# Performance work log

Measured on AMD Instinct MI355X. Metric: run time of the kernel, lower is better.

The kernel has to match this reference:

```python
import jax, jax.numpy as jnp
import numpy as np

B, S, D_IN, D_K, D_OUT = 8, 2048, 1024, 64, 64

def setup_inputs() -> dict:
    key = jax.random.key(0)
    k1, k2, k3, k4 = jax.random.split(key, 4)
    sc = 1.0 / np.sqrt(D_IN)
    return {
        "X": jax.random.normal(k1, (B, S, D_IN), dtype=jnp.float32),
        "Wq": jax.random.normal(k2, (D_IN, D_K), dtype=jnp.float32) * sc,
        "Wk": jax.random.normal(k3, (D_IN, D_K), dtype=jnp.float32) * sc,
        "Wv": jax.random.normal(k4, (D_IN, D_OUT), dtype=jnp.float32) * sc,
    }

def reference(X, Wq, Wk, Wv):
    # projections (no bias)
    Q = jnp.einsum('bsd,dk->bsk', X, Wq)   # [B,S,d_k]
    K = jnp.einsum('bsd,dk->bsk', X, Wk)   # [B,S,d_k]
    V = jnp.einsum('bsd,dv->bsv', X, Wv)   # [B,S,d_out]
    d_k = Q.shape[-1]
    S_mat = jnp.einsum('bqk,bsk->bqs', Q, K) / jnp.sqrt(jnp.float32(d_k))
    # causal mask: positions j > i get -inf
    causal = jnp.tril(jnp.ones((X.shape[1], X.shape[1]), dtype=bool))
    S_mat = jnp.where(causal[None, :, :], S_mat, -jnp.inf)
    A = jax.nn.softmax(S_mat, axis=-1)
    return jnp.einsum('bqs,bsv->bqv', A, V)
```

## Files before the change

kernel.cpp:

```cpp
#include <hip/hip_runtime.h>
#include <hip/hip_bf16.h>
#include <cstdint>
#include <cstddef>

#define BATCH 8
#define SEQ   2048
#define DIN   1024

typedef float f32x4 __attribute__((ext_vector_type(4)));
typedef float f32x8 __attribute__((ext_vector_type(8)));
typedef __bf16 bf16x8 __attribute__((ext_vector_type(8)));
typedef unsigned short ushort8_t __attribute__((ext_vector_type(8)));

__device__ __forceinline__ unsigned short bfu(float f) {
  __bf16 h = (__bf16)f;
  return __builtin_bit_cast(unsigned short, h);
}

__device__ __forceinline__ bf16x8 cvt8pair(float4 a, float4 b) {
  f32x8 v;
  v[0] = a.x; v[1] = a.y; v[2] = a.z; v[3] = a.w;
  v[4] = b.x; v[5] = b.y; v[6] = b.z; v[7] = b.w;
  return __builtin_convertvector(v, bf16x8);
}

__global__ void pack_w(const float* __restrict__ Wq, const float* __restrict__ Wk,
                       const float* __restrict__ Wv, unsigned short* __restrict__ Wp) {
  const int t = blockIdx.x * blockDim.x + threadIdx.x;
  const int lane = t & 63;
  const int grp = t >> 6;
  const int ks = grp & 31;
  const int nt = grp >> 5;
  const int n = nt * 16 + (lane & 15);
  const int k0 = ks * 32 + ((lane >> 4) << 3);
  const float* W;
  int col;
  float scale = 1.0f;
  if (n < 64)       { W = Wq; col = n;       scale = 0.125f; }
  else if (n < 128) { W = Wk; col = n - 64;  }
  else              { W = Wv; col = n - 128; }
  ushort8_t out;
#pragma unroll
  for (int j = 0; j < 8; ++j)
    out[j] = bfu(W[(size_t)(k0 + j) * 64 + col] * scale);
  reinterpret_cast<ushort8_t*>(Wp)[t] = out;
}

__global__ __launch_bounds__(256) void qkv_gemm(
    const float* __restrict__ X, const unsigned short* __restrict__ Wp,
    unsigned short* __restrict__ Qb, unsigned short* __restrict__ Kb,
    unsigned short* __restrict__ Vt) {
  __shared__ ushort8_t Af[2048];

  const int tid = threadIdx.x;
  const int lane = tid & 63;
  const int wave = tid >> 6;
  const int l15 = lane & 15;
  const int quad = lane >> 4;
  const int m0 = blockIdx.x * 32;
  const int nt0 = wave * 3;

  const int sr = tid >> 3;
  const int sk = tid & 7;
  const float* xrow = X + (size_t)(m0 + sr) * DIN;

  const ushort8_t* wp = reinterpret_cast<const ushort8_t*>(Wp) + nt0 * 2048 + lane;
  ushort8_t breg[2][3];
#pragma unroll
  for (int p = 0; p < 2; ++p)
#pragma unroll
    for (int nt = 0; nt < 3; ++nt) breg[p][nt] = wp[p * 64 + nt * 2048];

  f32x4 acc[2][3];
#pragma unroll
  for (int mt = 0; mt < 2; ++mt)
#pragma unroll
    for (int nt = 0; nt < 3; ++nt) acc[mt][nt] = (f32x4){0.f, 0.f, 0.f, 0.f};

  for (int half = 0; half < 2; ++half) {
    const int ksbase = half * 16;
    if (half) __syncthreads();
#pragma unroll
    for (int p = 0; p < 2; ++p) {
      const int ksl = sk + p * 8;
      const float4* src =
          reinterpret_cast<const float4*>(xrow + (ksbase + ksl) * 32);
      float4 f[8];
#pragma unroll
      for (int i = 0; i < 8; ++i) f[i] = src[i];
#pragma unroll
      for (int q = 0; q < 4; ++q)
        Af[(ksl * 4 + q) * 32 + sr] =
            __builtin_bit_cast(ushort8_t, cvt8pair(f[q * 2], f[q * 2 + 1]));
    }
    __syncthreads();

    for (int ksl = 0; ksl < 16; ++ksl) {
      const int ks = ksbase + ksl;
      const int p = ks & 1;
      bf16x8 af0 = __builtin_bit_cast(bf16x8, Af[(ksl * 4 + quad) * 32 + l15]);
      bf16x8 af1 = __builtin_bit_cast(bf16x8, Af[(ksl * 4 + quad) * 32 + 16 + l15]);
      bf16x8 b0 = __builtin_bit_cast(bf16x8, breg[p][0]);
      bf16x8 b1 = __builtin_bit_cast(bf16x8, breg[p][1]);
      bf16x8 b2 = __builtin_bit_cast(bf16x8, breg[p][2]);
      if (ks < 30) {
#pragma unroll
        for (int nt = 0; nt < 3; ++nt)
          breg[p][nt] = wp[(ks + 2) * 64 + nt * 2048];
      }
      acc[0][0] = __builtin_amdgcn_mfma_f32_16x16x32_bf16(af0, b0, acc[0][0], 0, 0, 0);
      acc[0][1] = __builtin_amdgcn_mfma_f32_16x16x32_bf16(af0, b1, acc[0][1], 0, 0, 0);
      acc[0][2] = __builtin_amdgcn_mfma_f32_16x16x32_bf16(af0, b2, acc[0][2], 0, 0, 0);
      acc[1][0] = __builtin_amdgcn_mfma_f32_16x16x32_bf16(af1, b0, acc[1][0], 0, 0, 0);
      acc[1][1] = __builtin_amdgcn_mfma_f32_16x16x32_bf16(af1, b1, acc[1][1], 0, 0, 0);
      acc[1][2] = __builtin_amdgcn_mfma_f32_16x16x32_bf16(af1, b2, acc[1][2], 0, 0, 0);
    }
  }

#pragma unroll
  for (int mt = 0; mt < 2; ++mt) {
    const int srow = m0 + mt * 16 + quad * 4;
    const int b = srow >> 11;
    const int s = srow & 2047;
#pragma unroll
    for (int nt = 0; nt < 3; ++nt) {
      const f32x4 a = acc[mt][nt];
      const int n = (nt0 + nt) * 16 + l15;
      if (n < 64) {
#pragma unroll
        for (int r = 0; r < 4; ++r)
          Qb[(size_t)(srow + r) * 64 + n] = bfu(a[r]);
      } else if (n < 128) {
#pragma unroll
        for (int r = 0; r < 4; ++r)
          Kb[(size_t)(srow + r) * 64 + (n - 64)] = bfu(a[r]);
      } else {
        const int dv = n - 128;
        ushort4 t4;
        t4.x = bfu(a[0]); t4.y = bfu(a[1]);
        t4.z = bfu(a[2]); t4.w = bfu(a[3]);
        *reinterpret_cast<ushort4*>(Vt + (((size_t)(b * 64 + dv)) << 11) + s) = t4;
      }
    }
  }
}

__global__ __launch_bounds__(256) void flash_kernel(
    const unsigned short* __restrict__ Qb, const unsigned short* __restrict__ Kb,
    const unsigned short* __restrict__ Vt, float* __restrict__ Out) {
  __shared__ float Olds[4][2][16][68];
  __shared__ float Llds[4][2][16];
  __shared__ unsigned short Pf[4][2][2][512];

  const int tid = threadIdx.x;
  const int lane = tid & 63;
  const int wave = tid >> 6;
  const int l15 = lane & 15;
  const int quad = lane >> 4;

  const int g = blockIdx.x;
  const int batch = g & 7;
  const int qb = 63 - (g >> 3);
  const int q0 = qb * 32;
  const int n64 = (q0 + 95) >> 6;

  bf16x8 qf[2][2];
#pragma unroll
  for (int mt = 0; mt < 2; ++mt) {
    const ushort8_t* qp = reinterpret_cast<const ushort8_t*>(
        Qb + (size_t)(batch * SEQ + q0 + mt * 16 + l15) * 64);
    qf[mt][0] = __builtin_bit_cast(bf16x8, qp[quad]);
    qf[mt][1] = __builtin_bit_cast(bf16x8, qp[4 + quad]);
  }

  const ushort8_t* kbase = reinterpret_cast<const ushort8_t*>(
      Kb + (size_t)(batch * SEQ + l15) * 64);
  const unsigned short* vtb = Vt + ((size_t)(batch * 64) << 11);

  f32x4 o[2][4];
  float lacc[2][4];
#pragma unroll
  for (int mt = 0; mt < 2; ++mt)
#pragma unroll
    for (int i = 0; i < 4; ++i) {
      o[mt][i] = (f32x4){0.f, 0.f, 0.f, 0.f};
      lacc[mt][i] = 0.f;
    }

  ushort8_t kbuf[8];
  if (wave < n64) {
#pragma unroll
    for (int h = 0; h < 4; ++h) {
      const ushort8_t* kp = kbase + (size_t)(wave * 64 + h * 16) * 8;
      kbuf[h * 2] = kp[quad];
      kbuf[h * 2 + 1] = kp[4 + quad];
    }
  }

  for (int kt = wave; kt < n64; kt += 4) {
    const int k0 = kt * 64;
    f32x4 s[2][4];
#pragma unroll
    for (int h = 0; h < 4; ++h) {
      bf16x8 kf0 = __builtin_bit_cast(bf16x8, kbuf[h * 2]);
      bf16x8 kf1 = __builtin_bit_cast(bf16x8, kbuf[h * 2 + 1]);
#pragma unroll
      for (int mt = 0; mt < 2; ++mt) {
        f32x4 z = (f32x4){0.f, 0.f, 0.f, 0.f};
        z = __builtin_amdgcn_mfma_f32_16x16x32_bf16(qf[mt][0], kf0, z, 0, 0, 0);
        z = __builtin_amdgcn_mfma_f32_16x16x32_bf16(qf[mt][1], kf1, z, 0, 0, 0);
        s[mt][h] = z;
      }
    }
    {
      const int nk = (kt + 4 < n64) ? kt + 4 : n64 - 1;
#pragma unroll
      for (int h = 0; h < 4; ++h) {
        const ushort8_t* kp = kbase + (size_t)(nk * 64 + h * 16) * 8;
        kbuf[h * 2] = kp[quad];
        kbuf[h * 2 + 1] = kp[4 + quad];
      }
    }
    ushort8_t vbuf[8];
#pragma unroll
    for (int c = 0; c < 2; ++c)
#pragma unroll
      for (int nt = 0; nt < 4; ++nt)
        vbuf[c * 4 + nt] = reinterpret_cast<const ushort8_t*>(
            vtb + (((size_t)(nt * 16 + l15)) << 11) + k0 + c * 32)[quad];
    if (kt == n64 - 1) {
#pragma unroll
      for (int mt = 0; mt < 2; ++mt)
#pragma unroll
        for (int h = 0; h < 4; ++h) {
          const int col = k0 + h * 16 + l15;
#pragma unroll
          for (int r = 0; r < 4; ++r) {
            const int row = q0 + mt * 16 + quad * 4 + r;
            if (col > row) s[mt][h][r] = -INFINITY;
          }
        }
    }
#pragma unroll
    for (int mt = 0; mt < 2; ++mt) {
#pragma unroll
      for (int h = 0; h < 4; ++h) {
        const int c = h >> 1;
        const int lp = ((h & 1) * 2 + (l15 >> 3)) * 16 + quad * 4;
        const int j = l15 & 7;
#pragma unroll
        for (int r = 0; r < 4; ++r) {
          const float pv = __expf(s[mt][h][r]);
          lacc[mt][r] += pv;
          Pf[wave][mt][c][(lp + r) * 8 + j] = bfu(pv);
        }
      }
    }
#pragma unroll
    for (int c = 0; c < 2; ++c) {
      bf16x8 pfm[2];
#pragma unroll
      for (int mt = 0; mt < 2; ++mt)
        pfm[mt] = __builtin_bit_cast(bf16x8,
            reinterpret_cast<const ushort8_t*>(&Pf[wave][mt][c][0])[lane]);
#pragma unroll
      for (int nt = 0; nt < 4; ++nt) {
        bf16x8 vf = __builtin_bit_cast(bf16x8, vbuf[c * 4 + nt]);
#pragma unroll
        for (int mt = 0; mt < 2; ++mt)
          o[mt][nt] = __builtin_amdgcn_mfma_f32_16x16x32_bf16(pfm[mt], vf, o[mt][nt], 0, 0, 0);
      }
    }
  }

#pragma unroll
  for (int off = 1; off < 16; off <<= 1)
#pragma unroll
    for (int mt = 0; mt < 2; ++mt)
#pragma unroll
      for (int r = 0; r < 4; ++r)
        lacc[mt][r] += __shfl_xor(lacc[mt][r], off, 64);

#pragma unroll
  for (int mt = 0; mt < 2; ++mt) {
#pragma unroll
    for (int nt = 0; nt < 4; ++nt)
#pragma unroll
      for (int r = 0; r < 4; ++r)
        Olds[wave][mt][quad * 4 + r][nt * 16 + l15] = o[mt][nt][r];
    if (l15 == 0) {
#pragma unroll
      for (int r = 0; r < 4; ++r) Llds[wave][mt][quad * 4 + r] = lacc[mt][r];
    }
  }
  __syncthreads();

  const int col = tid & 63;
  const int r0 = tid >> 6;
#pragma unroll
  for (int row = r0; row < 32; row += 4) {
    const int mt = row >> 4;
    const int rr = row & 15;
    float lstar = 0.f, accv = 0.f;
#pragma unroll
    for (int w = 0; w < 4; ++w) {
      lstar += Llds[w][mt][rr];
      accv += Olds[w][mt][rr][col];
    }
    Out[(size_t)(batch * SEQ + q0 + row) * 64 + col] = accv / lstar;
  }
}

extern "C" void kernel_launch(void* const* d_in, const int* in_sizes, int n_in,
                              void* d_out, int out_size, void* d_ws, size_t ws_size,
                              hipStream_t stream) {
  const float* X  = (const float*)d_in[0];
  const float* Wq = (const float*)d_in[1];
  const float* Wk = (const float*)d_in[2];
  const float* Wv = (const float*)d_in[3];
  float* Out = (float*)d_out;

  char* ws = (char*)d_ws;
  unsigned short* Wp = (unsigned short*)ws;
  unsigned short* Qb = (unsigned short*)(ws + (400 << 10));
  unsigned short* Kb = (unsigned short*)(ws + (400 << 10) + (2 << 20));
  unsigned short* Vt = (unsigned short*)(ws + (400 << 10) + (4 << 20));

  pack_w<<<96, 256, 0, stream>>>(Wq, Wk, Wv, Wp);
  qkv_gemm<<<512, 256, 0, stream>>>(X, Wp, Qb, Kb, Vt);
  flash_kernel<<<512, 256, 0, stream>>>(Qb, Kb, Vt, Out);
}
```

Before: 138.7 us.

## Double-buffer X staging, transpose score MFMA, use exp2 with packed P stores

The QKV GEMM now loads the second half of X into registers while the first half is computed, using two LDS buffers. The flash kernel swaps the MFMA operands so each lane holds four consecutive keys for one query row. This allows exp2 with log2e folded into the Q scale, a single packed 8-byte P store per tile, and a scalar row-sum reduced across quads. It also adds occupancy hints via launch_bounds(256,2) and interleaves heavy and light causal blocks across the grid to balance load. These changes target LDS store traffic, exp cost, shuffle count and tail imbalance, at the cost of more register pressure in the GEMM.

```diff
diff --git a/kernel.cpp b/kernel.cpp
--- a/kernel.cpp
+++ b/kernel.cpp
@@ -9,6 +9,7 @@
 
 typedef float f32x4 __attribute__((ext_vector_type(4)));
 typedef float f32x8 __attribute__((ext_vector_type(8)));
+typedef __bf16 bf16x4 __attribute__((ext_vector_type(4)));
 typedef __bf16 bf16x8 __attribute__((ext_vector_type(8)));
 typedef unsigned short ushort8_t __attribute__((ext_vector_type(8)));
 
@@ -36,7 +37,7 @@
   const float* W;
   int col;
   float scale = 1.0f;
-  if (n < 64)       { W = Wq; col = n;       scale = 0.125f; }
+  if (n < 64)       { W = Wq; col = n;       scale = 0.18033688011112042f; }
   else if (n < 128) { W = Wk; col = n - 64;  }
   else              { W = Wv; col = n - 128; }
   ushort8_t out;
@@ -46,11 +47,11 @@
   reinterpret_cast<ushort8_t*>(Wp)[t] = out;
 }
 
-__global__ __launch_bounds__(256) void qkv_gemm(
+__global__ __launch_bounds__(256, 2) void qkv_gemm(
     const float* __restrict__ X, const unsigned short* __restrict__ Wp,
     unsigned short* __restrict__ Qb, unsigned short* __restrict__ Kb,
     unsigned short* __restrict__ Vt) {
-  __shared__ ushort8_t Af[2048];
+  __shared__ ushort8_t Af[2][2048];
 
   const int tid = threadIdx.x;
   const int lane = tid & 63;
@@ -77,29 +78,12 @@
 #pragma unroll
     for (int nt = 0; nt < 3; ++nt) acc[mt][nt] = (f32x4){0.f, 0.f, 0.f, 0.f};
 
-  for (int half = 0; half < 2; ++half) {
-    const int ksbase = half * 16;
-    if (half) __syncthreads();
-#pragma unroll
-    for (int p = 0; p < 2; ++p) {
-      const int ksl = sk + p * 8;
-      const float4* src =
-          reinterpret_cast<const float4*>(xrow + (ksbase + ksl) * 32);
-      float4 f[8];
-#pragma unroll
-      for (int i = 0; i < 8; ++i) f[i] = src[i];
-#pragma unroll
-      for (int q = 0; q < 4; ++q)
-        Af[(ksl * 4 + q) * 32 + sr] =
-            __builtin_bit_cast(ushort8_t, cvt8pair(f[q * 2], f[q * 2 + 1]));
-    }
-    __syncthreads();
-
+  auto compute_half = [&](int ksbase, const ushort8_t* A) {
     for (int ksl = 0; ksl < 16; ++ksl) {
       const int ks = ksbase + ksl;
       const int p = ks & 1;
-      bf16x8 af0 = __builtin_bit_cast(bf16x8, Af[(ksl * 4 + quad) * 32 + l15]);
-      bf16x8 af1 = __builtin_bit_cast(bf16x8, Af[(ksl * 4 + quad) * 32 + 16 + l15]);
+      bf16x8 af0 = __builtin_bit_cast(bf16x8, A[(ksl * 4 + quad) * 32 + l15]);
+      bf16x8 af1 = __builtin_bit_cast(bf16x8, A[(ksl * 4 + quad) * 32 + 16 + l15]);
       bf16x8 b0 = __builtin_bit_cast(bf16x8, breg[p][0]);
       bf16x8 b1 = __builtin_bit_cast(bf16x8, breg[p][1]);
       bf16x8 b2 = __builtin_bit_cast(bf16x8, breg[p][2]);
@@ -115,7 +99,45 @@
       acc[1][1] = __builtin_amdgcn_mfma_f32_16x16x32_bf16(af1, b1, acc[1][1], 0, 0, 0);
       acc[1][2] = __builtin_amdgcn_mfma_f32_16x16x32_bf16(af1, b2, acc[1][2], 0, 0, 0);
     }
-  }
+  };
+
+  float4 xbuf[16];
+#pragma unroll
+  for (int p = 0; p < 2; ++p) {
+    const float4* src = reinterpret_cast<const float4*>(xrow + (sk + p * 8) * 32);
+#pragma unroll
+    for (int i = 0; i < 8; ++i) xbuf[p * 8 + i] = src[i];
+  }
+#pragma unroll
+  for (int p = 0; p < 2; ++p) {
+    const int ksl = sk + p * 8;
+#pragma unroll
+    for (int q = 0; q < 4; ++q)
+      Af[0][(ksl * 4 + q) * 32 + sr] =
+          __builtin_bit_cast(ushort8_t, cvt8pair(xbuf[p * 8 + q * 2], xbuf[p * 8 + q * 2 + 1]));
+  }
+  __syncthreads();
+
+#pragma unroll
+  for (int p = 0; p < 2; ++p) {
+    const float4* src = reinterpret_cast<const float4*>(xrow + (16 + sk + p * 8) * 32);
+#pragma unroll
+    for (int i = 0; i < 8; ++i) xbuf[p * 8 + i] = src[i];
+  }
+
+  compute_half(0, Af[0]);
+
+#pragma unroll
+  for (int p = 0; p < 2; ++p) {
+    const int ksl = sk + p * 8;
+#pragma unroll
+    for (int q = 0; q < 4; ++q)
+      Af[1][(ksl * 4 + q) * 32 + sr] =
+          __builtin_bit_cast(ushort8_t, cvt8pair(xbuf[p * 8 + q * 2], xbuf[p * 8 + q * 2 + 1]));
+  }
+  __syncthreads();
+
+  compute_half(16, Af[1]);
 
 #pragma unroll
   for (int mt = 0; mt < 2; ++mt) {
@@ -145,12 +167,12 @@
   }
 }
 
-__global__ __launch_bounds__(256) void flash_kernel(
+__global__ __launch_bounds__(256, 2) void flash_kernel(
     const unsigned short* __restrict__ Qb, const unsigned short* __restrict__ Kb,
     const unsigned short* __restrict__ Vt, float* __restrict__ Out) {
   __shared__ float Olds[4][2][16][68];
   __shared__ float Llds[4][2][16];
-  __shared__ unsigned short Pf[4][2][2][512];
+  __shared__ __attribute__((aligned(16))) unsigned short Pf[4][2][2][512];
 
   const int tid = threadIdx.x;
   const int lane = tid & 63;
@@ -160,7 +182,8 @@
 
   const int g = blockIdx.x;
   const int batch = g & 7;
-  const int qb = 63 - (g >> 3);
+  const int jj = (g >> 3) & 31;
+  const int qb = (g < 256) ? (63 - jj) : jj;
   const int q0 = qb * 32;
   const int n64 = (q0 + 95) >> 6;
 
@@ -177,15 +200,16 @@
       Kb + (size_t)(batch * SEQ + l15) * 64);
   const unsigned short* vtb = Vt + ((size_t)(batch * 64) << 11);
 
+  const int pbase = l15 * 8 + (quad >> 1) * 128 + (quad & 1) * 4;
+
   f32x4 o[2][4];
-  float lacc[2][4];
-#pragma unroll
-  for (int mt = 0; mt < 2; ++mt)
-#pragma unroll
-    for (int i = 0; i < 4; ++i) {
-      o[mt][i] = (f32x4){0.f, 0.f, 0.f, 0.f};
-      lacc[mt][i] = 0.f;
-    }
+  float lacc[2];
+#pragma unroll
+  for (int mt = 0; mt < 2; ++mt) {
+    lacc[mt] = 0.f;
+#pragma unroll
+    for (int i = 0; i < 4; ++i) o[mt][i] = (f32x4){0.f, 0.f, 0.f, 0.f};
+  }
 
   ushort8_t kbuf[8];
   if (wave < n64) {
@@ -207,8 +231,8 @@
 #pragma unroll
       for (int mt = 0; mt < 2; ++mt) {
         f32x4 z = (f32x4){0.f, 0.f, 0.f, 0.f};
-        z = __builtin_amdgcn_mfma_f32_16x16x32_bf16(qf[mt][0], kf0, z, 0, 0, 0);
-        z = __builtin_amdgcn_mfma_f32_16x16x32_bf16(qf[mt][1], kf1, z, 0, 0, 0);
+        z = __builtin_amdgcn_mfma_f32_16x16x32_bf16(kf0, qf[mt][0], z, 0, 0, 0);
+        z = __builtin_amdgcn_mfma_f32_16x16x32_bf16(kf1, qf[mt][1], z, 0, 0, 0);
         s[mt][h] = z;
       }
     }
@@ -230,30 +254,29 @@
             vtb + (((size_t)(nt * 16 + l15)) << 11) + k0 + c * 32)[quad];
     if (kt == n64 - 1) {
 #pragma unroll
-      for (int mt = 0; mt < 2; ++mt)
+      for (int mt = 0; mt < 2; ++mt) {
+        const int row = q0 + mt * 16 + l15;
 #pragma unroll
         for (int h = 0; h < 4; ++h) {
-          const int col = k0 + h * 16 + l15;
-#pragma unroll
-          for (int r = 0; r < 4; ++r) {
-            const int row = q0 + mt * 16 + quad * 4 + r;
-            if (col > row) s[mt][h][r] = -INFINITY;
-          }
+          const int colb = k0 + h * 16 + quad * 4;
+#pragma unroll
+          for (int r = 0; r < 4; ++r)
+            if (colb + r > row) s[mt][h][r] = -INFINITY;
         }
+      }
     }
 #pragma unroll
     for (int mt = 0; mt < 2; ++mt) {
 #pragma unroll
       for (int h = 0; h < 4; ++h) {
-        const int c = h >> 1;
-        const int lp = ((h & 1) * 2 + (l15 >> 3)) * 16 + quad * 4;
-        const int j = l15 & 7;
-#pragma unroll
-        for (int r = 0; r < 4; ++r) {
-          const float pv = __expf(s[mt][h][r]);
-          lacc[mt][r] += pv;
-          Pf[wave][mt][c][(lp + r) * 8 + j] = bfu(pv);
-        }
+        f32x4 p;
+#pragma unroll
+        for (int r = 0; r < 4; ++r) p[r] = __builtin_amdgcn_exp2f(s[mt][h][r]);
+        lacc[mt] += (p[0] + p[1]) + (p[2] + p[3]);
+        bf16x4 pk = __builtin_convertvector(p, bf16x4);
+        *reinterpret_cast<unsigned long long*>(
+            &Pf[wave][mt][h >> 1][pbase + ((h & 1) << 8)]) =
+            __builtin_bit_cast(unsigned long long, pk);
       }
     }
 #pragma unroll
@@ -274,12 +297,10 @@
   }
 
 #pragma unroll
-  for (int off = 1; off < 16; off <<= 1)
+  for (int off = 16; off < 64; off <<= 1)
 #pragma unroll
     for (int mt = 0; mt < 2; ++mt)
-#pragma unroll
-      for (int r = 0; r < 4; ++r)
-        lacc[mt][r] += __shfl_xor(lacc[mt][r], off, 64);
+      lacc[mt] += __shfl_xor(lacc[mt], off, 64);
 
 #pragma unroll
   for (int mt = 0; mt < 2; ++mt) {
@@ -288,10 +309,7 @@
 #pragma unroll
       for (int r = 0; r < 4; ++r)
         Olds[wave][mt][quad * 4 + r][nt * 16 + l15] = o[mt][nt][r];
-    if (l15 == 0) {
-#pragma unroll
-      for (int r = 0; r < 4; ++r) Llds[wave][mt][quad * 4 + r] = lacc[mt][r];
-    }
+    if (quad == 0) Llds[wave][mt][l15] = lacc[mt];
   }
   __syncthreads();
 
```

Result: faster. 133.5 us (-3.7%).
